# Kernel tuning notes

Hardware: AMD Instinct MI355X
Metric: run time of the kernel (lower is better)

## Reference

```python
import jax, jax.numpy as jnp
import numpy as np

N_NODES = 100000
N_EDGES = 1600000
NUM_GRAPHS = 128
ATOM_IN = 92
FEA = 64          # atom_fea_len
EDGE_DIM = 41
Z_DIM = 2 * FEA + EDGE_DIM  # 169, CGConv concat [x_i, x_j, edge_attr]
N_CONV = 5
HID = 256
LATENT = 128
CH = 3
BN_EPS = 1e-5


def setup_inputs() -> dict:
    key = jax.random.key(0)
    ks = jax.random.split(key, 16)
    x = jax.random.normal(ks[0], (N_NODES, ATOM_IN), dtype=jnp.float32)
    edge_index = jax.random.randint(ks[1], (2, N_EDGES), 0, N_NODES, dtype=jnp.int64)
    edge_attr = jax.random.uniform(ks[2], (N_EDGES, EDGE_DIM), dtype=jnp.float32)
    batch = jnp.sort(jax.random.randint(ks[3], (N_NODES,), 0, NUM_GRAPHS, dtype=jnp.int64))

    def lin(k, fan_in, fan_out):
        kw, kb = jax.random.split(k)
        bound = 1.0 / np.sqrt(fan_in)
        W = jax.random.uniform(kw, (fan_in, fan_out), jnp.float32, -bound, bound)
        b = jax.random.uniform(kb, (fan_out,), jnp.float32, -bound, bound)
        return W, b

    emb_W, emb_b = lin(ks[4], ATOM_IN, FEA)
    # stacked per-layer CGConv params: [N_CONV, ...]
    fW, fb, sW, sb = [], [], [], []
    for i in range(N_CONV):
        Wf, bf = lin(jax.random.fold_in(ks[5], i), Z_DIM, FEA)
        Ws, bs = lin(jax.random.fold_in(ks[6], i), Z_DIM, FEA)
        fW.append(Wf); fb.append(bf); sW.append(Ws); sb.append(bs)
    lin_f_W = jnp.stack(fW); lin_f_b = jnp.stack(fb)
    lin_s_W = jnp.stack(sW); lin_s_b = jnp.stack(sb)
    bn_gamma = jnp.ones((N_CONV, FEA), jnp.float32)
    bn_beta = jnp.zeros((N_CONV, FEA), jnp.float32)

    head_W1, head_b1 = lin(ks[7], FEA, HID)
    head_W2, head_b2 = lin(ks[8], HID, HID)
    head_W3, head_b3 = lin(ks[9], HID, LATENT * CH)
    return dict(x=x, edge_index=edge_index, edge_attr=edge_attr, batch=batch,
                emb_W=emb_W, emb_b=emb_b,
                lin_f_W=lin_f_W, lin_f_b=lin_f_b, lin_s_W=lin_s_W, lin_s_b=lin_s_b,
                bn_gamma=bn_gamma, bn_beta=bn_beta,
                head_W1=head_W1, head_b1=head_b1, head_W2=head_W2, head_b2=head_b2,
                head_W3=head_W3, head_b3=head_b3)


def _cgconv(h, src, dst, edge_attr, Wf, bf, Ws, bs, gamma, beta):
    # PyG CGConv: z = cat([x_i, x_j, edge_attr]); msg = sigmoid(lin_f(z)) * softplus(lin_s(z))
    # aggr='add' at target i (= edge_index[1]); batch_norm (training stats); residual.
    z = jnp.concatenate([h[dst], h[src], edge_attr], axis=-1)  # [E, 169]
    msg = jax.nn.sigmoid(z @ Wf + bf) * jax.nn.softplus(z @ Ws + bs)  # [E, 64]
    agg = jax.ops.segment_sum(msg, dst, num_segments=h.shape[0])  # [N, 64]
    mu = agg.mean(axis=0)
    var = agg.var(axis=0)  # biased, as in torch BN normalization
    out = (agg - mu) * jax.lax.rsqrt(var + BN_EPS) * gamma + beta
    return out + h


def reference(x, edge_index, edge_attr, batch,
              emb_W, emb_b, lin_f_W, lin_f_b, lin_s_W, lin_s_b, bn_gamma, bn_beta,
              head_W1, head_b1, head_W2, head_b2, head_W3, head_b3):
    src, dst = edge_index[0], edge_index[1]  # x_j = source, x_i = target
    h = x @ emb_W + emb_b  # [N, 64]
    for i in range(N_CONV):
        h = _cgconv(h, src, dst, edge_attr,
                    lin_f_W[i], lin_f_b[i], lin_s_W[i], lin_s_b[i],
                    bn_gamma[i], bn_beta[i])
    # global_mean_pool over graphs
    sums = jax.ops.segment_sum(h, batch, num_segments=NUM_GRAPHS)
    cnts = jax.ops.segment_sum(jnp.ones((h.shape[0],), h.dtype), batch, num_segments=NUM_GRAPHS)
    pooled = sums / jnp.maximum(cnts, 1.0)[:, None]  # [G, 64]
    g = jax.nn.softplus(pooled @ head_W1 + head_b1)
    g = jax.nn.softplus(g @ head_W2 + head_b2)
    dos = g @ head_W3 + head_b3  # [G, 384]
    return dos.reshape(-1, CH, LATENT)
```

## Files before the change

### kernel.cpp

```cpp
#include <hip/hip_runtime.h>
#include <math.h>

#define N_NODES 100000
#define N_EDGES 1600000
#define NUM_GRAPHS 128
#define ATOM_IN 92
#define FEA 64
#define EDGE_DIM 41
#define ZDIM 169
#define KPAD 192
#define EASTR 48
#define N_CONV 5
#define HID 256
#define OUT_PER_G 384
#define NPAD 100096
#define NBLK 391
#define ESTRIDE 200

#define HBYTES ((size_t)N_NODES * FEA * 4)

typedef __attribute__((ext_vector_type(8))) short bf16x8;
typedef __attribute__((ext_vector_type(4))) float f32x4;

__device__ __forceinline__ float sigmoidf_(float x) {
    return __builtin_amdgcn_rcpf(1.0f + __expf(-x));
}
__device__ __forceinline__ float softplusf_(float x) {
    float a = fabsf(x);
    return fmaxf(x, 0.0f) + __logf(1.0f + __expf(-a));
}
__device__ __forceinline__ unsigned short f2bf(float f) {
    unsigned int u = __float_as_uint(f);
    u = (u + 0x7FFFu + ((u >> 16) & 1u)) >> 16;
    return (unsigned short)u;
}

__global__ __launch_bounds__(256) void k_embed(const float* __restrict__ x,
                                               const float* __restrict__ W,
                                               const float* __restrict__ b,
                                               float* __restrict__ h,
                                               unsigned short* __restrict__ hb) {
    int idx = blockIdx.x * 256 + threadIdx.x;
    int c = idx & 63;
    int n = __builtin_amdgcn_readfirstlane(idx >> 6);
    float acc = 0.0f;
#pragma unroll 4
    for (int k = 0; k < ATOM_IN; ++k)
        acc = fmaf(x[n * ATOM_IN + k], W[k * FEA + c], acc);
    acc += b[c];
    h[idx] = acc;
    hb[idx] = f2bf(acc);
}

__global__ __launch_bounds__(256) void k_hist(const int* __restrict__ dst,
                                              int* __restrict__ cnt,
                                              int* __restrict__ rank) {
    int e = blockIdx.x * 256 + threadIdx.x;
    if (e < N_EDGES) rank[e] = atomicAdd(&cnt[dst[e]], 1);
}

__global__ __launch_bounds__(256) void k_blocksum(const int* __restrict__ cnt,
                                                  int* __restrict__ bsum) {
    __shared__ int s[256];
    int t = threadIdx.x;
    s[t] = cnt[blockIdx.x * 256 + t];
    __syncthreads();
    for (int o = 128; o > 0; o >>= 1) {
        if (t < o) s[t] += s[t + o];
        __syncthreads();
    }
    if (t == 0) bsum[blockIdx.x] = s[0];
}

__global__ __launch_bounds__(512) void k_topscan(int* __restrict__ bsum) {
    __shared__ int s[512];
    int t = threadIdx.x;
    int v = (t < NBLK) ? bsum[t] : 0;
    s[t] = v;
    __syncthreads();
    for (int o = 1; o < 512; o <<= 1) {
        int x = (t >= o) ? s[t - o] : 0;
        __syncthreads();
        s[t] += x;
        __syncthreads();
    }
    if (t < NBLK) bsum[t] = s[t] - v;
}

__global__ __launch_bounds__(256) void k_localscan(const int* __restrict__ cnt,
                                                   const int* __restrict__ bsum,
                                                   int* __restrict__ offs) {
    __shared__ int s[256];
    int t = threadIdx.x;
    int i = blockIdx.x * 256 + t;
    int v = cnt[i];
    s[t] = v;
    __syncthreads();
    for (int o = 1; o < 256; o <<= 1) {
        int x = (t >= o) ? s[t - o] : 0;
        __syncthreads();
        s[t] += x;
        __syncthreads();
    }
    offs[i] = bsum[blockIdx.x] + s[t] - v;
}

__global__ __launch_bounds__(256) void k_filldst(const int* __restrict__ offs,
                                                 const int* __restrict__ cnt,
                                                 int* __restrict__ dstS) {
    int n = blockIdx.x * 256 + threadIdx.x;
    int p = offs[n];
    for (int e = cnt[n]; e > 0; --e) dstS[p++] = n;
}

__global__ __launch_bounds__(256) void k_scatter_idx(const int* __restrict__ dst,
                                                     const int* __restrict__ src,
                                                     const int* __restrict__ offs,
                                                     const int* __restrict__ rank,
                                                     int* __restrict__ srcS,
                                                     int* __restrict__ eidS) {
    int e = blockIdx.x * 256 + threadIdx.x;
    int d = dst[e];
    int p = offs[d] + rank[e];
    srcS[p] = src[e];
    eidS[p] = e;
}

__global__ __launch_bounds__(256) void k_ea_gather(const float* __restrict__ ea,
                                                   const int* __restrict__ eidS,
                                                   unsigned short* __restrict__ eaSb) {
    __shared__ unsigned short sm[256 * EASTR];
    int t = threadIdx.x;
    int base = blockIdx.x * 256;
    int row = t >> 3, j = t & 7;
#pragma unroll
    for (int i = 0; i < 8; ++i) {
        int r = row + i * 32;
        int eid = eidS[base + r];
        const float* srcp = ea + (size_t)eid * EDGE_DIM;
#pragma unroll
        for (int cb = 0; cb < 6; ++cb) {
            int col = j + cb * 8;
            unsigned short v;
            if (col < EDGE_DIM)       v = f2bf(srcp[col]);
            else if (col == EDGE_DIM) v = 0x3F80;
            else                      v = 0;
            sm[r * EASTR + col] = v;
        }
    }
    __syncthreads();
    const uint4* s4 = (const uint4*)sm;
    uint4* d4 = (uint4*)(eaSb + (size_t)base * EASTR);
    for (int i = t; i < 256 * EASTR * 2 / 16; i += 256) d4[i] = s4[i];
}

__global__ __launch_bounds__(256) void k_wprep(const float* __restrict__ lfW,
                                               const float* __restrict__ lsW,
                                               const float* __restrict__ lfB,
                                               const float* __restrict__ lsB,
                                               unsigned short* __restrict__ WbT) {
    int idx = blockIdx.x * 256 + threadIdx.x;
    if (idx >= N_CONV * 128 * KPAD) return;
    int k = idx % KPAD;
    int c = (idx / KPAD) % 128;
    int L = idx / (KPAD * 128);
    float v = 0.0f;
    if (k < ZDIM) {
        const float* W = ((c < 64) ? lfW : lsW) + (size_t)L * ZDIM * FEA;
        v = W[k * FEA + (c & 63)];
    } else if (k == ZDIM) {
        v = ((c < 64) ? lfB : lsB)[L * FEA + (c & 63)];
    }
    WbT[idx] = f2bf(v);
}

__global__ __launch_bounds__(256) void k_edge(const unsigned short* __restrict__ hb,
                                              const int* __restrict__ dstS,
                                              const int* __restrict__ srcS,
                                              const unsigned short* __restrict__ eaSb,
                                              const unsigned short* __restrict__ WbT,
                                              float* __restrict__ agg) {
    __shared__ unsigned short z[64 * ESTRIDE];
    __shared__ int dsh[64];
    float* msg = (float*)z;

    int t = threadIdx.x;
    int l = t & 63;
    int w = t >> 6;
    int eb = blockIdx.x * 64;

    if (t < 64) dsh[t] = dstS[eb + t];

    {
        int e0 = (w << 3) + (l >> 3);
        int j = l & 7;
        int d0 = dstS[eb + e0], d1 = dstS[eb + e0 + 32];
        int s0 = srcS[eb + e0], s1 = srcS[eb + e0 + 32];
        *(uint4*)&z[e0 * ESTRIDE + j * 8] =
            *(const uint4*)&hb[(size_t)d0 * 64 + j * 8];
        *(uint4*)&z[(e0 + 32) * ESTRIDE + j * 8] =
            *(const uint4*)&hb[(size_t)d1 * 64 + j * 8];
        *(uint4*)&z[e0 * ESTRIDE + 64 + j * 8] =
            *(const uint4*)&hb[(size_t)s0 * 64 + j * 8];
        *(uint4*)&z[(e0 + 32) * ESTRIDE + 64 + j * 8] =
            *(const uint4*)&hb[(size_t)s1 * 64 + j * 8];
        if (j < 6) {
            *(uint4*)&z[e0 * ESTRIDE + 128 + j * 8] =
                *(const uint4*)&eaSb[(size_t)(eb + e0) * EASTR + j * 8];
            *(uint4*)&z[(e0 + 32) * ESTRIDE + 128 + j * 8] =
                *(const uint4*)&eaSb[(size_t)(eb + e0 + 32) * EASTR + j * 8];
        } else {
            uint4 zr = make_uint4(0u, 0u, 0u, 0u);
            *(uint4*)&z[e0 * ESTRIDE + 128 + j * 8] = zr;
            *(uint4*)&z[(e0 + 32) * ESTRIDE + 128 + j * 8] = zr;
        }
    }
    __syncthreads();

    int lm = l & 15, lg = l >> 4;
    int col = w * 16 + lm;
    const unsigned short* WF = WbT + (size_t)col * KPAD;
    const unsigned short* WS = WbT + (size_t)(64 + col) * KPAD;
    f32x4 accF[4] = {};
    f32x4 accS[4] = {};
#pragma unroll
    for (int ks = 0; ks < 6; ++ks) {
        int kofs = ks * 32 + lg * 8;
        bf16x8 a[4];
#pragma unroll
        for (int r = 0; r < 4; ++r)
            a[r] = *(const bf16x8*)&z[(16 * r + lm) * ESTRIDE + kofs];
        bf16x8 bF = *(const bf16x8*)&WF[kofs];
        bf16x8 bS = *(const bf16x8*)&WS[kofs];
#pragma unroll
        for (int r = 0; r < 4; ++r) {
            accF[r] = __builtin_amdgcn_mfma_f32_16x16x32_bf16(a[r], bF, accF[r], 0, 0, 0);
            accS[r] = __builtin_amdgcn_mfma_f32_16x16x32_bf16(a[r], bS, accS[r], 0, 0, 0);
        }
    }
    __syncthreads();

#pragma unroll
    for (int r = 0; r < 4; ++r)
#pragma unroll
        for (int j = 0; j < 4; ++j) {
            int e = 16 * r + 4 * lg + j;
            msg[e * 66 + col] = sigmoidf_(accF[r][j]) * softplusf_(accS[r][j]);
        }
    __syncthreads();

    {
        int e0 = w * 16;
        bool bnd = (l < 15) && (dsh[e0 + l] != dsh[e0 + l + 1]);
        unsigned long long bm = __ballot(bnd) | (1ull << 15);
        float a = 0.0f;
#pragma unroll
        for (int i = 0; i < 16; ++i) {
            a += msg[(e0 + i) * 66 + l];
            if (bm & (1ull << i)) {
                atomicAdd(&agg[(size_t)dsh[e0 + i] * FEA + l], a);
                a = 0.0f;
            }
        }
    }
}

__global__ __launch_bounds__(256) void k_bnstats(const float* __restrict__ agg,
                                                 float* __restrict__ stats) {
    int t = threadIdx.x, c = t & 63, w = t >> 6;
    int r0 = blockIdx.x * 100;
    float s = 0.0f, q = 0.0f;
    for (int r = r0 + w; r < r0 + 100; r += 4) {
        float v = agg[(size_t)r * FEA + c];
        s += v;
        q = fmaf(v, v, q);
    }
    __shared__ float red[2][256];
    red[0][t] = s;
    red[1][t] = q;
    __syncthreads();
    if (t < 64) {
        s = red[0][t] + red[0][t + 64] + red[0][t + 128] + red[0][t + 192];
        q = red[1][t] + red[1][t + 64] + red[1][t + 128] + red[1][t + 192];
        atomicAdd(&stats[t], s);
        atomicAdd(&stats[64 + t], q);
    }
}

__global__ __launch_bounds__(256) void k_bnapply(float* __restrict__ agg,
                                                 const float* __restrict__ stats,
                                                 const float* __restrict__ gamma,
                                                 const float* __restrict__ beta,
                                                 float* __restrict__ h,
                                                 unsigned short* __restrict__ hb) {
    const size_t total4 = (size_t)N_NODES * FEA / 4;
    for (size_t i4 = (size_t)blockIdx.x * 256 + threadIdx.x; i4 < total4;
         i4 += (size_t)gridDim.x * 256) {
        size_t idx = i4 * 4;
        int c0 = (int)(idx & 63);
        float4 v = *(float4*)&agg[idx];
        *(float4*)&agg[idx] = make_float4(0.f, 0.f, 0.f, 0.f);
        float4 hv = *(float4*)&h[idx];
        float o[4];
        unsigned short ob[4];
#pragma unroll
        for (int k = 0; k < 4; ++k) {
            int c = c0 + k;
            float mu = stats[c] * (1.0f / N_NODES);
            float var = stats[64 + c] * (1.0f / N_NODES) - mu * mu;
            float rs = rsqrtf(var + 1e-5f);
            float vk = (k == 0) ? v.x : (k == 1) ? v.y : (k == 2) ? v.z : v.w;
            float hk = (k == 0) ? hv.x : (k == 1) ? hv.y : (k == 2) ? hv.z : hv.w;
            float hn = hk + (vk - mu) * rs * gamma[c] + beta[c];
            o[k] = hn;
            ob[k] = f2bf(hn);
        }
        *(float4*)&h[idx] = make_float4(o[0], o[1], o[2], o[3]);
        *(uint2*)&hb[idx] = *(uint2*)ob;
    }
}

__global__ __launch_bounds__(256) void k_pool(const float* __restrict__ h,
                                              const int* __restrict__ batch,
                                              float* __restrict__ psum,
                                              float* __restrict__ pcnt) {
    int g = blockIdx.x;
    int lo, hi;
    {
        int a = 0, b = N_NODES;
        while (a < b) { int m = (a + b) >> 1; if (batch[m] < g) a = m + 1; else b = m; }
        lo = a;
    }
    {
        int a = lo, b = N_NODES;
        while (a < b) { int m = (a + b) >> 1; if (batch[m] < g + 1) a = m + 1; else b = m; }
        hi = a;
    }
    int t = threadIdx.x, c = t & 63, w = t >> 6;
    float s = 0.0f;
    for (int r = lo + w; r < hi; r += 4) s += h[(size_t)r * FEA + c];
    __shared__ float red[256];
    red[t] = s;
    __syncthreads();
    if (t < 64) {
        psum[g * FEA + t] = red[t] + red[t + 64] + red[t + 128] + red[t + 192];
        if (t == 0) pcnt[g] = (float)(hi - lo);
    }
}

__global__ __launch_bounds__(256) void k_head(const float* __restrict__ psum,
                                              const float* __restrict__ pcnt,
                                              const float* __restrict__ W1, const float* __restrict__ b1,
                                              const float* __restrict__ W2, const float* __restrict__ b2,
                                              const float* __restrict__ W3, const float* __restrict__ b3,
                                              float* __restrict__ out) {
    int g = blockIdx.x, t = threadIdx.x;
    __shared__ float p[64], g1[256], g2[256];
    if (t < 64) p[t] = psum[g * FEA + t] / fmaxf(pcnt[g], 1.0f);
    __syncthreads();
    {
        float acc = b1[t];
#pragma unroll 8
        for (int k = 0; k < FEA; ++k) acc = fmaf(p[k], W1[k * HID + t], acc);
        g1[t] = softplusf_(acc);
    }
    __syncthreads();
    {
        float acc = b2[t];
#pragma unroll 8
        for (int k = 0; k < HID; ++k) acc = fmaf(g1[k], W2[k * HID + t], acc);
        g2[t] = softplusf_(acc);
    }
    __syncthreads();
    for (int c = t; c < OUT_PER_G; c += 256) {
        float acc = b3[c];
#pragma unroll 8
        for (int k = 0; k < HID; ++k) acc = fmaf(g2[k], W3[k * OUT_PER_G + c], acc);
        out[g * OUT_PER_G + c] = acc;
    }
}

extern "C" void kernel_launch(void* const* d_in, const int* in_sizes, int n_in,
                              void* d_out, int out_size, void* d_ws, size_t ws_size,
                              hipStream_t stream) {
    (void)in_sizes; (void)n_in; (void)out_size; (void)ws_size;
    const float* x    = (const float*)d_in[0];
    const int*   ei   = (const int*)d_in[1];
    const float* ea   = (const float*)d_in[2];
    const int*   batch= (const int*)d_in[3];
    const float* embW = (const float*)d_in[4];
    const float* embB = (const float*)d_in[5];
    const float* lfW  = (const float*)d_in[6];
    const float* lfB  = (const float*)d_in[7];
    const float* lsW  = (const float*)d_in[8];
    const float* lsB  = (const float*)d_in[9];
    const float* gam  = (const float*)d_in[10];
    const float* bet  = (const float*)d_in[11];
    const float* W1 = (const float*)d_in[12];
    const float* b1 = (const float*)d_in[13];
    const float* W2 = (const float*)d_in[14];
    const float* b2 = (const float*)d_in[15];
    const float* W3 = (const float*)d_in[16];
    const float* b3 = (const float*)d_in[17];

    const int* srcI = ei;
    const int* dstI = ei + N_EDGES;

    char* ws = (char*)d_ws;
    size_t off = 0;
    float* h      = (float*)(ws + off); off += HBYTES;
    float* agg    = (float*)(ws + off); off += HBYTES;
    float* stats  = (float*)(ws + off); off += 5 * 512;
    float* psum   = (float*)(ws + off); off += 32768;
    float* pcnt   = (float*)(ws + off); off += 512;
    unsigned short* hbuf = (unsigned short*)(ws + off); off += (size_t)N_NODES * 64 * 2;
    unsigned short* eaSb = (unsigned short*)(ws + off); off += (size_t)N_EDGES * EASTR * 2;
    unsigned short* WbT  = (unsigned short*)(ws + off); off += (size_t)N_CONV * 128 * KPAD * 2;
    int*   cnt    = (int*)(ws + off);   off += (size_t)NPAD * 4;
    int*   bsum   = (int*)(ws + off);   off += 2048;
    int*   offs   = (int*)(ws + off);   off += (size_t)NPAD * 4;
    int*   rank   = (int*)(ws + off);   off += (size_t)N_EDGES * 4;
    int*   dstS   = (int*)(ws + off);   off += (size_t)N_EDGES * 4;
    int*   srcS   = (int*)(ws + off);   off += (size_t)N_EDGES * 4;
    int*   eidS   = (int*)(ws + off);   off += (size_t)N_EDGES * 4;

    hipMemsetAsync(cnt, 0, (size_t)NPAD * 4, stream);
    k_hist<<<(N_EDGES + 255) / 256, 256, 0, stream>>>(dstI, cnt, rank);
    k_blocksum<<<NBLK, 256, 0, stream>>>(cnt, bsum);
    k_topscan<<<1, 512, 0, stream>>>(bsum);
    k_localscan<<<NBLK, 256, 0, stream>>>(cnt, bsum, offs);
    k_filldst<<<NBLK, 256, 0, stream>>>(offs, cnt, dstS);
    k_scatter_idx<<<N_EDGES / 256, 256, 0, stream>>>(dstI, srcI, offs, rank,
                                                     srcS, eidS);
    k_ea_gather<<<N_EDGES / 256, 256, 0, stream>>>(ea, eidS, eaSb);
    k_wprep<<<(N_CONV * 128 * KPAD + 255) / 256, 256, 0, stream>>>(lfW, lsW,
                                                                   lfB, lsB, WbT);

    k_embed<<<N_NODES * FEA / 256, 256, 0, stream>>>(x, embW, embB, h, hbuf);

    hipMemsetAsync(agg, 0, HBYTES + 5 * 512, stream);

    for (int L = 0; L < N_CONV; ++L) {
        k_edge<<<N_EDGES / 64, 256, 0, stream>>>(hbuf, dstS, srcS, eaSb,
                                                 WbT + (size_t)L * 128 * KPAD,
                                                 agg);
        k_bnstats<<<1000, 256, 0, stream>>>(agg, stats + L * 128);
        k_bnapply<<<2048, 256, 0, stream>>>(agg, stats + L * 128,
                                            gam + L * FEA, bet + L * FEA,
                                            h, hbuf);
    }

    k_pool<<<NUM_GRAPHS, 256, 0, stream>>>(h, batch, psum, pcnt);
    k_head<<<NUM_GRAPHS, 256, 0, stream>>>(psum, pcnt, W1, b1, W2, b2, W3, b3,
                                           (float*)d_out);
}
```

Measured before the change: 1.570 ms.

## Process two edge tiles per block with register-prefetched gather of next tile

The edge kernel now handles 128 edges per block in two 64-edge tiles, staging gathered node and edge features in registers. The second tile's global gathers are issued before the first tile's MFMA compute, so their latency overlaps with compute and the atomic scatter. The launch bound also requests 6 blocks per CU, which caps register use. The cost is extra registers for the prefetch buffers and extra barriers, which can reduce occupancy or cause spills, and half as many blocks are launched.

New measurement: 2.295 ms. +46.2%, slower.

```diff
diff --git a/kernel.cpp b/kernel.cpp
--- a/kernel.cpp
+++ b/kernel.cpp
@@ -174,12 +174,12 @@
     WbT[idx] = f2bf(v);
 }
 
-__global__ __launch_bounds__(256) void k_edge(const unsigned short* __restrict__ hb,
-                                              const int* __restrict__ dstS,
-                                              const int* __restrict__ srcS,
-                                              const unsigned short* __restrict__ eaSb,
-                                              const unsigned short* __restrict__ WbT,
-                                              float* __restrict__ agg) {
+__global__ __launch_bounds__(256, 6) void k_edge(const unsigned short* __restrict__ hb,
+                                                 const int* __restrict__ dstS,
+                                                 const int* __restrict__ srcS,
+                                                 const unsigned short* __restrict__ eaSb,
+                                                 const unsigned short* __restrict__ WbT,
+                                                 float* __restrict__ agg) {
     __shared__ unsigned short z[64 * ESTRIDE];
     __shared__ int dsh[64];
     float* msg = (float*)z;
@@ -187,80 +187,106 @@
     int t = threadIdx.x;
     int l = t & 63;
     int w = t >> 6;
-    int eb = blockIdx.x * 64;
-
-    if (t < 64) dsh[t] = dstS[eb + t];
-
-    {
-        int e0 = (w << 3) + (l >> 3);
-        int j = l & 7;
-        int d0 = dstS[eb + e0], d1 = dstS[eb + e0 + 32];
-        int s0 = srcS[eb + e0], s1 = srcS[eb + e0 + 32];
-        *(uint4*)&z[e0 * ESTRIDE + j * 8] =
-            *(const uint4*)&hb[(size_t)d0 * 64 + j * 8];
-        *(uint4*)&z[(e0 + 32) * ESTRIDE + j * 8] =
-            *(const uint4*)&hb[(size_t)d1 * 64 + j * 8];
-        *(uint4*)&z[e0 * ESTRIDE + 64 + j * 8] =
-            *(const uint4*)&hb[(size_t)s0 * 64 + j * 8];
-        *(uint4*)&z[(e0 + 32) * ESTRIDE + 64 + j * 8] =
-            *(const uint4*)&hb[(size_t)s1 * 64 + j * 8];
-        if (j < 6) {
-            *(uint4*)&z[e0 * ESTRIDE + 128 + j * 8] =
-                *(const uint4*)&eaSb[(size_t)(eb + e0) * EASTR + j * 8];
-            *(uint4*)&z[(e0 + 32) * ESTRIDE + 128 + j * 8] =
-                *(const uint4*)&eaSb[(size_t)(eb + e0 + 32) * EASTR + j * 8];
-        } else {
-            uint4 zr = make_uint4(0u, 0u, 0u, 0u);
-            *(uint4*)&z[e0 * ESTRIDE + 128 + j * 8] = zr;
-            *(uint4*)&z[(e0 + 32) * ESTRIDE + 128 + j * 8] = zr;
-        }
-    }
-    __syncthreads();
-
     int lm = l & 15, lg = l >> 4;
     int col = w * 16 + lm;
+    int e0 = (w << 3) + (l >> 3);
+    int j = l & 7;
     const unsigned short* WF = WbT + (size_t)col * KPAD;
     const unsigned short* WS = WbT + (size_t)(64 + col) * KPAD;
-    f32x4 accF[4] = {};
-    f32x4 accS[4] = {};
-#pragma unroll
-    for (int ks = 0; ks < 6; ++ks) {
-        int kofs = ks * 32 + lg * 8;
-        bf16x8 a[4];
+
+    int ebA = blockIdx.x * 128;
+
+    uint4 r0, r1, r2, r3, r4, r5;
+    {
+        int d0 = dstS[ebA + e0], d1 = dstS[ebA + e0 + 32];
+        int s0 = srcS[ebA + e0], s1 = srcS[ebA + e0 + 32];
+        r0 = *(const uint4*)&hb[(size_t)d0 * 64 + j * 8];
+        r1 = *(const uint4*)&hb[(size_t)d1 * 64 + j * 8];
+        r2 = *(const uint4*)&hb[(size_t)s0 * 64 + j * 8];
+        r3 = *(const uint4*)&hb[(size_t)s1 * 64 + j * 8];
+        if (j < 6) {
+            r4 = *(const uint4*)&eaSb[(size_t)(ebA + e0) * EASTR + j * 8];
+            r5 = *(const uint4*)&eaSb[(size_t)(ebA + e0 + 32) * EASTR + j * 8];
+        } else {
+            r4 = make_uint4(0u, 0u, 0u, 0u);
+            r5 = make_uint4(0u, 0u, 0u, 0u);
+        }
+    }
+    if (t < 64) dsh[t] = dstS[ebA + t];
+    int dshB = (t < 64) ? dstS[ebA + 64 + t] : 0;
+
+#pragma unroll
+    for (int tile = 0; tile < 2; ++tile) {
+        *(uint4*)&z[e0 * ESTRIDE + j * 8] = r0;
+        *(uint4*)&z[(e0 + 32) * ESTRIDE + j * 8] = r1;
+        *(uint4*)&z[e0 * ESTRIDE + 64 + j * 8] = r2;
+        *(uint4*)&z[(e0 + 32) * ESTRIDE + 64 + j * 8] = r3;
+        *(uint4*)&z[e0 * ESTRIDE + 128 + j * 8] = r4;
+        *(uint4*)&z[(e0 + 32) * ESTRIDE + 128 + j * 8] = r5;
+
+        if (tile == 0) {
+            int ebB = ebA + 64;
+            int d0 = dstS[ebB + e0], d1 = dstS[ebB + e0 + 32];
+            int s0 = srcS[ebB + e0], s1 = srcS[ebB + e0 + 32];
+            r0 = *(const uint4*)&hb[(size_t)d0 * 64 + j * 8];
+            r1 = *(const uint4*)&hb[(size_t)d1 * 64 + j * 8];
+            r2 = *(const uint4*)&hb[(size_t)s0 * 64 + j * 8];
+            r3 = *(const uint4*)&hb[(size_t)s1 * 64 + j * 8];
+            if (j < 6) {
+                r4 = *(const uint4*)&eaSb[(size_t)(ebB + e0) * EASTR + j * 8];
+                r5 = *(const uint4*)&eaSb[(size_t)(ebB + e0 + 32) * EASTR + j * 8];
+            }
+        }
+        __syncthreads();
+
+        f32x4 accF[4] = {};
+        f32x4 accS[4] = {};
+#pragma unroll
+        for (int ks = 0; ks < 6; ++ks) {
+            int kofs = ks * 32 + lg * 8;
+            bf16x8 a[4];
+#pragma unroll
+            for (int r = 0; r < 4; ++r)
+                a[r] = *(const bf16x8*)&z[(16 * r + lm) * ESTRIDE + kofs];
+            bf16x8 bF = *(const bf16x8*)&WF[kofs];
+            bf16x8 bS = *(const bf16x8*)&WS[kofs];
+#pragma unroll
+            for (int r = 0; r < 4; ++r) {
+                accF[r] = __builtin_amdgcn_mfma_f32_16x16x32_bf16(a[r], bF, accF[r], 0, 0, 0);
+                accS[r] = __builtin_amdgcn_mfma_f32_16x16x32_bf16(a[r], bS, accS[r], 0, 0, 0);
+            }
+        }
+        __syncthreads();
+
 #pragma unroll
         for (int r = 0; r < 4; ++r)
-            a[r] = *(const bf16x8*)&z[(16 * r + lm) * ESTRIDE + kofs];
-        bf16x8 bF = *(const bf16x8*)&WF[kofs];
-        bf16x8 bS = *(const bf16x8*)&WS[kofs];
-#pragma unroll
-        for (int r = 0; r < 4; ++r) {
-            accF[r] = __builtin_amdgcn_mfma_f32_16x16x32_bf16(a[r], bF, accF[r], 0, 0, 0);
-            accS[r] = __builtin_amdgcn_mfma_f32_16x16x32_bf16(a[r], bS, accS[r], 0, 0, 0);
-        }
-    }
-    __syncthreads();
-
-#pragma unroll
-    for (int r = 0; r < 4; ++r)
-#pragma unroll
-        for (int j = 0; j < 4; ++j) {
-            int e = 16 * r + 4 * lg + j;
-            msg[e * 66 + col] = sigmoidf_(accF[r][j]) * softplusf_(accS[r][j]);
-        }
-    __syncthreads();
-
-    {
-        int e0 = w * 16;
-        bool bnd = (l < 15) && (dsh[e0 + l] != dsh[e0 + l + 1]);
-        unsigned long long bm = __ballot(bnd) | (1ull << 15);
-        float a = 0.0f;
-#pragma unroll
-        for (int i = 0; i < 16; ++i) {
-            a += msg[(e0 + i) * 66 + l];
-            if (bm & (1ull << i)) {
-                atomicAdd(&agg[(size_t)dsh[e0 + i] * FEA + l], a);
-                a = 0.0f;
+#pragma unroll
+            for (int jj = 0; jj < 4; ++jj) {
+                int e = 16 * r + 4 * lg + jj;
+                msg[e * 66 + col] = sigmoidf_(accF[r][jj]) * softplusf_(accS[r][jj]);
             }
+        __syncthreads();
+
+        {
+            int ee0 = w * 16;
+            int eb = ebA + tile * 64;
+            bool bnd = (l < 15) && (dsh[ee0 + l] != dsh[ee0 + l + 1]);
+            unsigned long long bm = __ballot(bnd) | (1ull << 15);
+            float a = 0.0f;
+#pragma unroll
+            for (int i = 0; i < 16; ++i) {
+                a += msg[(ee0 + i) * 66 + l];
+                if (bm & (1ull << i)) {
+                    atomicAdd(&agg[(size_t)dsh[ee0 + i] * FEA + l], a);
+                    a = 0.0f;
+                }
+            }
+            (void)eb;
+        }
+
+        if (tile == 0) {
+            __syncthreads();
+            if (t < 64) dsh[t] = dshB;
         }
     }
 }
@@ -441,9 +467,9 @@
     hipMemsetAsync(agg, 0, HBYTES + 5 * 512, stream);
 
     for (int L = 0; L < N_CONV; ++L) {
-        k_edge<<<N_EDGES / 64, 256, 0, stream>>>(hbuf, dstS, srcS, eaSb,
-                                                 WbT + (size_t)L * 128 * KPAD,
-                                                 agg);
+        k_edge<<<N_EDGES / 128, 256, 0, stream>>>(hbuf, dstS, srcS, eaSb,
+                                                  WbT + (size_t)L * 128 * KPAD,
+                                                  agg);
         k_bnstats<<<1000, 256, 0, stream>>>(agg, stats + L * 128);
         k_bnapply<<<2048, 256, 0, stream>>>(agg, stats + L * 128,
                                             gam + L * FEA, bet + L * FEA,
```
